# Kernel optimization log

Hardware: AMD Instinct MI355X
Metric: run time of the kernel (lower is better)

## Reference

```python
import jax, jax.numpy as jnp
import numpy as np

B, S, D, H = 8, 1024, 512, 12
HS = D // H  # 42 (head_size; 12*42 = 504 concat width, as in the original)


def setup_inputs() -> dict:
    key = jax.random.key(0)
    ks = jax.random.split(key, 12)
    sd = 0.02
    return {
        "embedded_patches": jax.random.normal(ks[0], (B, S, D), dtype=jnp.float32),
        # stacked per-head projections (12 independent Linear(D, HS, bias=False))
        "wk": jax.random.normal(ks[1], (H, D, HS), dtype=jnp.float32) * sd,
        "wq": jax.random.normal(ks[2], (H, D, HS), dtype=jnp.float32) * sd,
        "wv": jax.random.normal(ks[3], (H, D, HS), dtype=jnp.float32) * sd,
        "w_proj": jax.random.normal(ks[4], (H * HS, D), dtype=jnp.float32) * sd,  # [504, 512]
        "b_proj": jnp.zeros((D,), dtype=jnp.float32),
        # shared LayerNorm (same params used for both norms, as in the original)
        "gamma": jnp.ones((D,), dtype=jnp.float32),
        "beta": jnp.zeros((D,), dtype=jnp.float32),
        "w1": jax.random.normal(ks[5], (D, 4 * D), dtype=jnp.float32) * sd,
        "b1": jnp.zeros((4 * D,), dtype=jnp.float32),
        "w2": jax.random.normal(ks[6], (4 * D, D), dtype=jnp.float32) * sd,
        "b2": jnp.zeros((D,), dtype=jnp.float32),
    }


def _layernorm(x, gamma, beta, eps=1e-5):
    mu = jnp.mean(x, axis=-1, keepdims=True)
    var = jnp.var(x, axis=-1, keepdims=True)
    return (x - mu) * jax.lax.rsqrt(var + eps) * gamma + beta


def reference(embedded_patches, wk, wq, wv, w_proj, b_proj, gamma, beta, w1, b1, w2, b2):
    x = embedded_patches
    n1 = _layernorm(x, gamma, beta)
    # per-head projections, vectorized over heads: [B,S,D] x [H,D,E] -> [B,H,S,E]
    q = jnp.einsum('bsd,hde->bhse', n1, wq)
    k = jnp.einsum('bsd,hde->bhse', n1, wk)
    v = jnp.einsum('bsd,hde->bhse', n1, wv)
    scale = HS ** -0.5
    wei = jax.nn.softmax(jnp.einsum('bhse,bhte->bhst', q, k) * scale, axis=-1)
    out = jnp.einsum('bhst,bhte->bhse', wei, v)        # [B,H,S,E]
    out = out.transpose(0, 2, 1, 3).reshape(B, S, H * HS)  # concat heads -> [B,S,504]
    attn = out @ w_proj + b_proj                       # [B,S,D]
    # original quirk: takes batch element 0 and broadcasts against residual
    first_added = attn[0] + x                          # [S,D] + [B,S,D] -> [B,S,D]
    n2 = _layernorm(first_added, gamma, beta)
    h = jax.nn.gelu(n2 @ w1 + b1, approximate=False)   # torch nn.GELU default = exact erf
    ff = h @ w2 + b2
    return ff + first_added
```

## Files before the change

### kernel.cpp

```cpp
#include <hip/hip_runtime.h>
#include <hip/hip_bf16.h>
#include <stdint.h>


typedef unsigned short u16;
typedef __attribute__((ext_vector_type(8))) short short8;
typedef __attribute__((ext_vector_type(4))) float f32x4;

__device__ __forceinline__ u16 f2bf(float f) {
  union { float f; unsigned u; } x; x.f = f;
  return (u16)((x.u + 0x7FFFu + ((x.u >> 16) & 1u)) >> 16);
}
__device__ __forceinline__ float bf2f(u16 u) {
  union { unsigned u; float f; } x; x.u = ((unsigned)u) << 16;
  return x.f;
}

__device__ __forceinline__ void gload_lds16(const u16* g, u16* l) {
  __builtin_amdgcn_global_load_lds(
      (__attribute__((address_space(1))) void*)g,
      (__attribute__((address_space(3))) void*)l, 16, 0, 0);
}

__device__ __forceinline__ float wred_sum(float v) {
#pragma unroll
  for (int off = 32; off > 0; off >>= 1) v += __shfl_xor(v, off, 64);
  return v;
}
__device__ __forceinline__ float wred_max(float v) {
#pragma unroll
  for (int off = 32; off > 0; off >>= 1) v = fmaxf(v, __shfl_xor(v, off, 64));
  return v;
}

#define MFMA16x16(a, b, c) __builtin_amdgcn_mfma_f32_16x16x32_bf16(a, b, c, 0, 0, 0)

enum { EP_BF16 = 0, EP_PV = 1, EP_F32B = 2, EP_GELU = 3, EP_OUT = 4,
       EP_PART = 5, EP_PVPART = 6 };

template <int EP>
__launch_bounds__(256, 4)
__global__ void gemm2(const u16* __restrict__ A, int lda, long sAz,
                      const u16* __restrict__ Bt, int ldb, long sBz,
                      void* __restrict__ Cv, int ldc, long sCz,
                      int K, const float* __restrict__ bias,
                      const float* __restrict__ aux) {
  __shared__ u16 lA[2][128 * 32];
  __shared__ u16 lB[2][128 * 32];
  const int z = blockIdx.z;
  const u16* Ab;
  const u16* Bb;
  if (EP == EP_PVPART) {
    Ab = A + (long)(z >> 2) * sAz + (z & 3) * 256;
    Bb = Bt + (long)(z >> 2) * sBz + (z & 3) * 256;
  } else {
    Ab = A + (long)z * sAz;
    Bb = Bt + (long)z * sBz;
  }
  const int m0 = blockIdx.x * 128;
  const int n0 = blockIdx.y * 128;
  const int tid = threadIdx.x;
  const int w = tid >> 6;
  const int l = tid & 63;
  const int wr = w >> 1;
  const int wc = w & 1;
  const int NT = K >> 5;

  f32x4 acc[4][4];
#pragma unroll
  for (int i = 0; i < 4; ++i)
#pragma unroll
    for (int j = 0; j < 4; ++j) acc[i][j] = (f32x4){0.f, 0.f, 0.f, 0.f};

  const int srow = w * 32 + (l >> 2);
  const int sk = ((l & 3) ^ ((l >> 3) & 3)) * 8;
  const u16* ga0 = Ab + (long)(m0 + srow) * lda + sk;
  const u16* ga1 = Ab + (long)(m0 + srow + 16) * lda + sk;
  const u16* gb0 = Bb + (long)(n0 + srow) * ldb + sk;
  const u16* gb1 = Bb + (long)(n0 + srow + 16) * ldb + sk;
  const int dOff = w * 1024;

  const int gphys = ((l >> 4) ^ ((l >> 1) & 3)) * 8;
  const int aoff = (wr * 64 + (l & 15)) * 32 + gphys;
  const int boff = (wc * 64 + (l & 15)) * 32 + gphys;

  gload_lds16(ga0, &lA[0][dOff]);
  gload_lds16(ga1, &lA[0][dOff + 512]);
  gload_lds16(gb0, &lB[0][dOff]);
  gload_lds16(gb1, &lB[0][dOff + 512]);
  __syncthreads();

  int buf = 0;
  for (int t = 0; t < NT; ++t) {
    short8 af[4], bfv[4];
#pragma unroll
    for (int mi = 0; mi < 4; ++mi)
      af[mi] = *(const short8*)&lA[buf][aoff + mi * 16 * 32];
#pragma unroll
    for (int ni = 0; ni < 4; ++ni)
      bfv[ni] = *(const short8*)&lB[buf][boff + ni * 16 * 32];
    if (t + 1 < NT) {
      const int k0 = (t + 1) * 32;
      const int nb = buf ^ 1;
      gload_lds16(ga0 + k0, &lA[nb][dOff]);
      gload_lds16(ga1 + k0, &lA[nb][dOff + 512]);
      gload_lds16(gb0 + k0, &lB[nb][dOff]);
      gload_lds16(gb1 + k0, &lB[nb][dOff + 512]);
    }
#pragma unroll
    for (int mi = 0; mi < 4; ++mi)
#pragma unroll
      for (int ni = 0; ni < 4; ++ni)
        acc[mi][ni] = MFMA16x16(af[mi], bfv[ni], acc[mi][ni]);
    __syncthreads();
    buf ^= 1;
  }

  const int rbase = m0 + wr * 64 + (l >> 4) * 4;
  const int cbase = n0 + wc * 64 + (l & 15);
#pragma unroll
  for (int mi = 0; mi < 4; ++mi) {
#pragma unroll
    for (int ni = 0; ni < 4; ++ni) {
#pragma unroll
      for (int j = 0; j < 4; ++j) {
        const int row = rbase + mi * 16 + j;
        const int col = cbase + ni * 16;
        const float v = acc[mi][ni][j];
        if (EP == EP_BF16) {
          ((u16*)Cv)[(long)z * sCz + (long)row * ldc + col] = f2bf(v);
        } else if (EP == EP_PV) {
          if (col < 42) {
            const float iv = aux[z * 1024 + row];
            ((u16*)Cv)[(long)row * ldc + z * 42 + col] = f2bf(v * iv);
          }
        } else if (EP == EP_F32B) {
          ((float*)Cv)[(long)row * ldc + col] = v + bias[col];
        } else if (EP == EP_GELU) {
          const float tt = v + bias[col];
          const float g = 0.5f * tt * (1.0f + erff(tt * 0.70710678118654752f));
          ((u16*)Cv)[(long)row * ldc + col] = f2bf(g);
        } else if (EP == EP_OUT) {
          ((float*)Cv)[(long)row * ldc + col] =
              v + bias[col] + aux[(long)row * ldc + col];
        } else {
          ((float*)Cv)[(long)z * sCz + (long)row * ldc + col] = v;
        }
      }
    }
  }
}

__global__ void combine_mlp2_kernel(const float* __restrict__ p,
                                    const float* __restrict__ fa,
                                    const float* __restrict__ b2,
                                    float* __restrict__ out) {
  const long i = (long)blockIdx.x * 256 + threadIdx.x;
  const f32x4 a = ((const f32x4*)p)[i];
  const f32x4 b = ((const f32x4*)(p + 8192L * 512))[i];
  const f32x4 f = ((const f32x4*)fa)[i];
  const f32x4 bb = ((const f32x4*)b2)[i & 127];
  ((f32x4*)out)[i] = a + b + f + bb;
}

__global__ void combine_pv_kernel(const float* __restrict__ part,
                                  const float* __restrict__ invl,
                                  u16* __restrict__ cat) {
  const int blk = blockIdx.x;
  const int h = blk >> 10;
  const int row = blk & 1023;
  const int e = threadIdx.x;
  if (e >= 42) return;
  const long base = (long)(h * 4) * 131072 + row * 128 + e;
  float v = part[base] + part[base + 131072] + part[base + 2 * 131072] +
            part[base + 3 * 131072];
  cat[(long)row * 512 + h * 42 + e] = f2bf(v * invl[h * 1024 + row]);
}

__global__ void ln1_kernel(const float* __restrict__ x,
                           const float* __restrict__ gamma,
                           const float* __restrict__ beta,
                           u16* __restrict__ n1) {
  __shared__ float red[16];
  const int s = blockIdx.x;
  const int t = threadIdx.x;
  const float* row = x + (long)s * 512;
  const float v0 = row[t];
  const float v1 = row[t + 256];
  float sum = wred_sum(v0 + v1);
  float sq = wred_sum(v0 * v0 + v1 * v1);
  if ((t & 63) == 0) { red[t >> 6] = sum; red[8 + (t >> 6)] = sq; }
  __syncthreads();
  sum = red[0] + red[1] + red[2] + red[3];
  sq = red[8] + red[9] + red[10] + red[11];
  const float mu = sum * (1.0f / 512.0f);
  const float rstd = rsqrtf(sq * (1.0f / 512.0f) - mu * mu + 1e-5f);
  n1[(long)s * 512 + t] = f2bf((v0 - mu) * rstd * gamma[t] + beta[t]);
  n1[(long)s * 512 + t + 256] =
      f2bf((v1 - mu) * rstd * gamma[t + 256] + beta[t + 256]);
}

__global__ void ln2_kernel(const float* __restrict__ x,
                           const float* __restrict__ aproj,
                           const float* __restrict__ gamma,
                           const float* __restrict__ beta,
                           float* __restrict__ fa, u16* __restrict__ n2) {
  __shared__ float red[16];
  const int r = blockIdx.x;
  const int t = threadIdx.x;
  const int s = r & 1023;
  const float* xr = x + (long)r * 512;
  const float* ar = aproj + (long)s * 512;
  const float v0 = xr[t] + ar[t];
  const float v1 = xr[t + 256] + ar[t + 256];
  fa[(long)r * 512 + t] = v0;
  fa[(long)r * 512 + t + 256] = v1;
  float sum = wred_sum(v0 + v1);
  float sq = wred_sum(v0 * v0 + v1 * v1);
  if ((t & 63) == 0) { red[t >> 6] = sum; red[8 + (t >> 6)] = sq; }
  __syncthreads();
  sum = red[0] + red[1] + red[2] + red[3];
  sq = red[8] + red[9] + red[10] + red[11];
  const float mu = sum * (1.0f / 512.0f);
  const float rstd = rsqrtf(sq * (1.0f / 512.0f) - mu * mu + 1e-5f);
  n2[(long)r * 512 + t] = f2bf((v0 - mu) * rstd * gamma[t] + beta[t]);
  n2[(long)r * 512 + t + 256] =
      f2bf((v1 - mu) * rstd * gamma[t + 256] + beta[t + 256]);
}

__global__ void softmax_kernel(u16* __restrict__ SP, float* __restrict__ invl) {
  __shared__ float red[16];
  const long row = blockIdx.x;
  u16* p = SP + row * 1024;
  const int t = threadIdx.x;
  uint2 u = ((const uint2*)p)[t];
  const float s0 = bf2f((u16)(u.x & 0xffff));
  const float s1 = bf2f((u16)(u.x >> 16));
  const float s2 = bf2f((u16)(u.y & 0xffff));
  const float s3 = bf2f((u16)(u.y >> 16));
  float m = wred_max(fmaxf(fmaxf(s0, s1), fmaxf(s2, s3)));
  if ((t & 63) == 0) red[t >> 6] = m;
  __syncthreads();
  m = fmaxf(fmaxf(red[0], red[1]), fmaxf(red[2], red[3]));
  const float e0 = __expf(s0 - m), e1 = __expf(s1 - m);
  const float e2 = __expf(s2 - m), e3 = __expf(s3 - m);
  float sum = wred_sum(e0 + e1 + e2 + e3);
  if ((t & 63) == 0) red[8 + (t >> 6)] = sum;
  __syncthreads();
  sum = red[8] + red[9] + red[10] + red[11];
  if (t == 0) invl[row] = 1.0f / sum;
  uint2 o;
  o.x = (unsigned)f2bf(e0) | ((unsigned)f2bf(e1) << 16);
  o.y = (unsigned)f2bf(e2) | ((unsigned)f2bf(e3) << 16);
  ((uint2*)p)[t] = o;
}

__global__ void prep_qkv_kernel(const float* __restrict__ wq,
                                const float* __restrict__ wk,
                                u16* __restrict__ BtQKV, float scale) {
  const int i = blockIdx.x * 256 + threadIdx.x;
  const int n = i >> 9, d = i & 511;
  const int pq = n / 768;
  const int h = (n % 768) >> 6;
  const int e = n & 63;
  float v = 0.f;
  if (e < 42) {
    v = (pq ? wk : wq)[((long)h * 512 + d) * 42 + e];
    if (!pq) v *= scale;
  }
  BtQKV[i] = f2bf(v);
}
__global__ void prep_wvT_kernel(const float* __restrict__ wv,
                                u16* __restrict__ wvT) {
  const int i = blockIdx.x * 256 + threadIdx.x;
  const int r = i >> 9, d = i & 511;
  const int h = r >> 7, e = r & 127;
  wvT[i] = f2bf(e < 42 ? wv[((long)h * 512 + d) * 42 + e] : 0.f);
}

__global__ void transpose_bf16_kernel(const float* __restrict__ in,
                                      u16* __restrict__ out, int N, int Kin,
                                      int Kpad) {
  __shared__ float tile[64][65];
  const int n0 = blockIdx.x * 64;
  const int k0 = blockIdx.y * 64;
  const int t = threadIdx.x;
  const int tc = t & 63;
  const int tr = t >> 6;
#pragma unroll
  for (int r = 0; r < 16; ++r) {
    const int kr = tr * 16 + r;
    const int kg = k0 + kr;
    tile[kr][tc] = (kg < Kin) ? in[(long)kg * N + n0 + tc] : 0.f;
  }
  __syncthreads();
  const int nr0 = t >> 4;
  const int kc = (t & 15) * 4;
#pragma unroll
  for (int p = 0; p < 4; ++p) {
    const int nr = nr0 + p * 16;
    ushort4 v;
    v.x = f2bf(tile[kc + 0][nr]);
    v.y = f2bf(tile[kc + 1][nr]);
    v.z = f2bf(tile[kc + 2][nr]);
    v.w = f2bf(tile[kc + 3][nr]);
    *(ushort4*)&out[(long)(n0 + nr) * Kpad + k0 + kc] = v;
  }
}

__global__ void zero_u16_kernel(u16* __restrict__ p) {
  p[blockIdx.x * 256 + threadIdx.x] = 0;
}

extern "C" void kernel_launch(void* const* d_in, const int* in_sizes, int n_in,
                              void* d_out, int out_size, void* d_ws,
                              size_t ws_size, hipStream_t stream) {
  const float* x = (const float*)d_in[0];
  const float* wk = (const float*)d_in[1];
  const float* wq = (const float*)d_in[2];
  const float* wv = (const float*)d_in[3];
  const float* w_proj = (const float*)d_in[4];
  const float* b_proj = (const float*)d_in[5];
  const float* gamma = (const float*)d_in[6];
  const float* beta = (const float*)d_in[7];
  const float* w1 = (const float*)d_in[8];
  const float* b1 = (const float*)d_in[9];
  const float* w2 = (const float*)d_in[10];
  const float* b2 = (const float*)d_in[11];

  char* base = (char*)d_ws;
  size_t off = 0;
  auto alloc = [&](size_t bytes) -> void* {
    void* p = base + off;
    off += (bytes + 255) & ~(size_t)255;
    return p;
  };
  u16* n1 = (u16*)alloc(1024L * 512 * 2);
  u16* qkvc = (u16*)alloc(1024L * 1536 * 2);
  u16* SP = (u16*)alloc(12L * 1024 * 1024 * 2);
  u16* wvT = (u16*)alloc(1536L * 512 * 2);
  u16* vt = (u16*)alloc(1536L * 1024 * 2);
  u16* cat = (u16*)alloc(1024L * 512 * 2);
  float* aproj = (float*)alloc(1024L * 512 * 4);
  float* fa = (float*)alloc(8192L * 512 * 4);
  u16* n2 = (u16*)alloc(8192L * 512 * 2);
  u16* hbuf = (u16*)alloc(8192L * 2048 * 2);
  u16* BtQKV = (u16*)alloc(1536L * 512 * 2);
  u16* BtP = (u16*)alloc(512L * 512 * 2);
  u16* Bt1 = (u16*)alloc(2048L * 512 * 2);
  u16* Bt2 = (u16*)alloc(512L * 2048 * 2);
  float* invl = (float*)alloc(12L * 1024 * 4);
  float* pvpart = (float*)alloc(48L * 1024 * 128 * 4);
  float* part = (float*)d_ws;
  (void)ws_size; (void)in_sizes; (void)n_in; (void)out_size;

  const float scale = 0.15430334996209191f;

  prep_qkv_kernel<<<3072, 256, 0, stream>>>(wq, wk, BtQKV, scale);
  prep_wvT_kernel<<<3072, 256, 0, stream>>>(wv, wvT);
  transpose_bf16_kernel<<<dim3(8, 8), 256, 0, stream>>>(w_proj, BtP, 512, 504, 512);
  transpose_bf16_kernel<<<dim3(32, 8), 256, 0, stream>>>(w1, Bt1, 2048, 512, 512);
  transpose_bf16_kernel<<<dim3(8, 32), 256, 0, stream>>>(w2, Bt2, 512, 2048, 2048);
  zero_u16_kernel<<<2048, 256, 0, stream>>>(cat);
  ln1_kernel<<<1024, 256, 0, stream>>>(x, gamma, beta, n1);

  gemm2<EP_BF16><<<dim3(8, 12, 1), 256, 0, stream>>>(
      n1, 512, 0, BtQKV, 512, 0, qkvc, 1536, 0, 512, nullptr, nullptr);
  gemm2<EP_BF16><<<dim3(12, 8, 1), 256, 0, stream>>>(
      wvT, 512, 0, n1, 512, 0, vt, 1024, 0, 512, nullptr, nullptr);
  gemm2<EP_BF16><<<dim3(8, 8, 12), 256, 0, stream>>>(
      qkvc, 1536, 64, qkvc + 768, 1536, 64, SP, 1024, 1024L * 1024, 64,
      nullptr, nullptr);
  softmax_kernel<<<12288, 256, 0, stream>>>(SP, invl);
  gemm2<EP_PVPART><<<dim3(8, 1, 48), 256, 0, stream>>>(
      SP, 1024, 1024L * 1024, vt, 1024, 128L * 1024, pvpart, 128,
      1024L * 128, 256, nullptr, nullptr);
  combine_pv_kernel<<<12288, 64, 0, stream>>>(pvpart, invl, cat);
  gemm2<EP_F32B><<<dim3(8, 4, 1), 256, 0, stream>>>(
      cat, 512, 0, BtP, 512, 0, aproj, 512, 0, 512, b_proj, nullptr);
  ln2_kernel<<<8192, 256, 0, stream>>>(x, aproj, gamma, beta, fa, n2);
  gemm2<EP_GELU><<<dim3(64, 16, 1), 256, 0, stream>>>(
      n2, 512, 0, Bt1, 512, 0, hbuf, 2048, 0, 512, b1, nullptr);
  gemm2<EP_PART><<<dim3(64, 4, 2), 256, 0, stream>>>(
      hbuf, 2048, 1024, Bt2, 2048, 1024, part, 512, 8192L * 512, 1024,
      nullptr, nullptr);
  combine_mlp2_kernel<<<4096, 256, 0, stream>>>(part, fa, b2, (float*)d_out);
}
```

Baseline: 185.1 us.

## Triple-buffer GEMM LDS pipeline with single barrier and explicit waitcnts

After: 180.7 us. 1.02x faster.

```diff
diff --git a/kernel.cpp b/kernel.cpp
--- a/kernel.cpp
+++ b/kernel.cpp
@@ -39,14 +39,13 @@
        EP_PART = 5, EP_PVPART = 6 };
 
 template <int EP>
-__launch_bounds__(256, 4)
-__global__ void gemm2(const u16* __restrict__ A, int lda, long sAz,
+__launch_bounds__(256, 3)
+__global__ void gemm3(const u16* __restrict__ A, int lda, long sAz,
                       const u16* __restrict__ Bt, int ldb, long sBz,
                       void* __restrict__ Cv, int ldc, long sCz,
                       int K, const float* __restrict__ bias,
                       const float* __restrict__ aux) {
-  __shared__ u16 lA[2][128 * 32];
-  __shared__ u16 lB[2][128 * 32];
+  __shared__ u16 lds[3][8192];
   const int z = blockIdx.z;
   const u16* Ab;
   const u16* Bb;
@@ -73,48 +72,58 @@
     for (int j = 0; j < 4; ++j) acc[i][j] = (f32x4){0.f, 0.f, 0.f, 0.f};
 
   const int srow = w * 32 + (l >> 2);
-  const int sk = ((l & 3) ^ ((l >> 3) & 3)) * 8;
+  const int sk = (l & 3) * 8;
   const u16* ga0 = Ab + (long)(m0 + srow) * lda + sk;
   const u16* ga1 = Ab + (long)(m0 + srow + 16) * lda + sk;
   const u16* gb0 = Bb + (long)(n0 + srow) * ldb + sk;
   const u16* gb1 = Bb + (long)(n0 + srow + 16) * ldb + sk;
-  const int dOff = w * 1024;
-
-  const int gphys = ((l >> 4) ^ ((l >> 1) & 3)) * 8;
-  const int aoff = (wr * 64 + (l & 15)) * 32 + gphys;
-  const int boff = (wc * 64 + (l & 15)) * 32 + gphys;
-
-  gload_lds16(ga0, &lA[0][dOff]);
-  gload_lds16(ga1, &lA[0][dOff + 512]);
-  gload_lds16(gb0, &lB[0][dOff]);
-  gload_lds16(gb1, &lB[0][dOff + 512]);
-  __syncthreads();
-
-  int buf = 0;
+  const int dA = w * 1024;
+  const int dB = 4096 + w * 1024;
+
+  const int aoff = (wr * 64 + (l & 15)) * 32 + (l >> 4) * 8;
+  const int boff = 4096 + (wc * 64 + (l & 15)) * 32 + (l >> 4) * 8;
+
+  u16* r0 = &lds[0][0];
+  u16* r1 = &lds[1][0];
+  u16* r2 = &lds[2][0];
+
+#define STAGE(dst, kt)                          \
+  do {                                          \
+    const int k0_ = (kt) * 32;                  \
+    gload_lds16(ga0 + k0_, (dst) + dA);         \
+    gload_lds16(ga1 + k0_, (dst) + dA + 512);   \
+    gload_lds16(gb0 + k0_, (dst) + dB);         \
+    gload_lds16(gb1 + k0_, (dst) + dB + 512);   \
+  } while (0)
+
+  STAGE(r0, 0);
+  STAGE(r1, 1);
+
   for (int t = 0; t < NT; ++t) {
+    asm volatile("s_waitcnt vmcnt(4)" ::: "memory");
+    __builtin_amdgcn_s_barrier();
+    __builtin_amdgcn_sched_barrier(0);
+    int t2 = t + 2;
+    if (t2 >= NT) t2 -= NT;
+    STAGE(r2, t2);
     short8 af[4], bfv[4];
 #pragma unroll
     for (int mi = 0; mi < 4; ++mi)
-      af[mi] = *(const short8*)&lA[buf][aoff + mi * 16 * 32];
+      af[mi] = *(const short8*)&r0[aoff + mi * 16 * 32];
 #pragma unroll
     for (int ni = 0; ni < 4; ++ni)
-      bfv[ni] = *(const short8*)&lB[buf][boff + ni * 16 * 32];
-    if (t + 1 < NT) {
-      const int k0 = (t + 1) * 32;
-      const int nb = buf ^ 1;
-      gload_lds16(ga0 + k0, &lA[nb][dOff]);
-      gload_lds16(ga1 + k0, &lA[nb][dOff + 512]);
-      gload_lds16(gb0 + k0, &lB[nb][dOff]);
-      gload_lds16(gb1 + k0, &lB[nb][dOff + 512]);
-    }
+      bfv[ni] = *(const short8*)&r0[boff + ni * 16 * 32];
+    asm volatile("s_waitcnt lgkmcnt(0)" ::: "memory");
+    __builtin_amdgcn_sched_barrier(0);
 #pragma unroll
     for (int mi = 0; mi < 4; ++mi)
 #pragma unroll
       for (int ni = 0; ni < 4; ++ni)
         acc[mi][ni] = MFMA16x16(af[mi], bfv[ni], acc[mi][ni]);
-    __syncthreads();
-    buf ^= 1;
-  }
+    u16* tmp = r0; r0 = r1; r1 = r2; r2 = tmp;
+  }
+  asm volatile("s_waitcnt vmcnt(0)" ::: "memory");
+#undef STAGE
 
   const int rbase = m0 + wr * 64 + (l >> 4) * 4;
   const int cbase = n0 + wc * 64 + (l & 15);
@@ -364,24 +373,24 @@
   zero_u16_kernel<<<2048, 256, 0, stream>>>(cat);
   ln1_kernel<<<1024, 256, 0, stream>>>(x, gamma, beta, n1);
 
-  gemm2<EP_BF16><<<dim3(8, 12, 1), 256, 0, stream>>>(
+  gemm3<EP_BF16><<<dim3(8, 12, 1), 256, 0, stream>>>(
       n1, 512, 0, BtQKV, 512, 0, qkvc, 1536, 0, 512, nullptr, nullptr);
-  gemm2<EP_BF16><<<dim3(12, 8, 1), 256, 0, stream>>>(
+  gemm3<EP_BF16><<<dim3(12, 8, 1), 256, 0, stream>>>(
       wvT, 512, 0, n1, 512, 0, vt, 1024, 0, 512, nullptr, nullptr);
-  gemm2<EP_BF16><<<dim3(8, 8, 12), 256, 0, stream>>>(
+  gemm3<EP_BF16><<<dim3(8, 8, 12), 256, 0, stream>>>(
       qkvc, 1536, 64, qkvc + 768, 1536, 64, SP, 1024, 1024L * 1024, 64,
       nullptr, nullptr);
   softmax_kernel<<<12288, 256, 0, stream>>>(SP, invl);
-  gemm2<EP_PVPART><<<dim3(8, 1, 48), 256, 0, stream>>>(
+  gemm3<EP_PVPART><<<dim3(8, 1, 48), 256, 0, stream>>>(
       SP, 1024, 1024L * 1024, vt, 1024, 128L * 1024, pvpart, 128,
       1024L * 128, 256, nullptr, nullptr);
   combine_pv_kernel<<<12288, 64, 0, stream>>>(pvpart, invl, cat);
-  gemm2<EP_F32B><<<dim3(8, 4, 1), 256, 0, stream>>>(
+  gemm3<EP_F32B><<<dim3(8, 4, 1), 256, 0, stream>>>(
       cat, 512, 0, BtP, 512, 0, aproj, 512, 0, 512, b_proj, nullptr);
   ln2_kernel<<<8192, 256, 0, stream>>>(x, aproj, gamma, beta, fa, n2);
-  gemm2<EP_GELU><<<dim3(64, 16, 1), 256, 0, stream>>>(
+  gemm3<EP_GELU><<<dim3(64, 16, 1), 256, 0, stream>>>(
       n2, 512, 0, Bt1, 512, 0, hbuf, 2048, 0, 512, b1, nullptr);
-  gemm2<EP_PART><<<dim3(64, 4, 2), 256, 0, stream>>>(
+  gemm3<EP_PART><<<dim3(64, 4, 2), 256, 0, stream>>>(
       hbuf, 2048, 1024, Bt2, 2048, 1024, part, 512, 8192L * 512, 1024,
       nullptr, nullptr);
   combine_mlp2_kernel<<<4096, 256, 0, stream>>>(part, fa, b2, (float*)d_out);
```
